# Optimization experiments

Hardware: AMD Instinct MI355X
Metric: run time of the kernel (lower is better)

The kernel has to match this reference:

```python
import jax, jax.numpy as jnp
import numpy as np

ENTRY_SIZE = 8192
TUPLE_SIZE = 16
N_NEURONS = ENTRY_SIZE // TUPLE_SIZE            # 512
ADDR_SPACE = 2 ** TUPLE_SIZE                     # 65536
BATCH = 4096


def setup_inputs() -> dict:
    key = jax.random.key(0)
    k1, k2, k3 = jax.random.split(key, 3)
    # Binary input bits [B, entry_size]
    inp = jax.random.randint(k1, (BATCH, ENTRY_SIZE), 0, 2, dtype=jnp.int32)
    # Permutation mapping bits -> tuples (identity permutation; arange fill)
    tuple_mapping = jnp.arange(ENTRY_SIZE, dtype=jnp.int64)
    # Dense RAM tables emulating the per-neuron dicts:
    #   counts[n, a] = number of training samples that hit address a in neuron n
    #                  (0 means the address was never trained -> not in dict)
    #   sums[n, a]   = accumulated target sum for that address
    counts = jax.random.randint(k2, (N_NEURONS, ADDR_SPACE), 0, 4, dtype=jnp.int32)
    sums = jax.random.normal(k3, (N_NEURONS, ADDR_SPACE), dtype=jnp.float32)
    return {"input": inp, "tuple_mapping": tuple_mapping, "counts": counts, "sums": sums}


def reference(input, tuple_mapping, counts, sums):
    """RegressionWisard.predict with centrality='mean'.

    input:  [B, entry_size] binary bits (int32)
    tuple_mapping: [entry_size] permutation (int)
    counts: [n_neurons, 2^tuple_size] int32 RAM hit counts
    sums:   [n_neurons, 2^tuple_size] float32 RAM target sums
    """
    B = input.shape[0]
    # Map and group bits into tuples: [B, N, T]
    mapped = jnp.take(input, tuple_mapping, axis=1).reshape(B, N_NEURONS, TUPLE_SIZE)
    # Binary address per (sample, neuron); tidx flips so bit 0 is the MSB.
    pow2 = (jnp.int32(1) << jnp.arange(TUPLE_SIZE - 1, -1, -1, dtype=jnp.int32))
    addr = jnp.einsum("bnt,t->bn", mapped, pow2)  # [B, N], values in [0, 2^T)
    neuron_idx = jnp.arange(N_NEURONS, dtype=jnp.int32)[None, :]  # [1, N]
    c = counts[neuron_idx, addr]  # [B, N]
    s = sums[neuron_idx, addr]    # [B, N]
    trained = c > 0               # dict-membership (torch.isin) equivalent
    response = jnp.sum(jnp.where(trained, s, jnp.float32(0)), axis=1)      # [B]
    counters = jnp.sum(jnp.where(trained, c, 0), axis=1).astype(s.dtype)   # [B]
    return jnp.nan_to_num(response / counters)
```

## Files before the change

kernel.cpp:

```cpp
#include <hip/hip_runtime.h>


constexpr int BATCH   = 4096;
constexpr int ENTRY   = 8192;
constexpr int TUP     = 16;
constexpr int NEUR    = ENTRY / TUP;
constexpr int THREADS = 256;
constexpr int SPB     = 2;
constexpr int KPT     = NEUR / THREADS;

typedef int v4i __attribute__((ext_vector_type(4)));

__global__ __launch_bounds__(THREADS) void wisard_kernel(
    const int*   __restrict__ input,
    const int*   __restrict__ mapping,
    const int*   __restrict__ counts,
    const float* __restrict__ sums,
    float*       __restrict__ out)
{
    __shared__ float s_resp[SPB][THREADS / 64];
    __shared__ int   s_cnt [SPB][THREADS / 64];

    const int tid  = threadIdx.x;
    const int lane = tid & 63;
    const int wv   = tid >> 6;
    const int b0   = blockIdx.x * SPB;

    int   cv[SPB][KPT];
    float sv[SPB][KPT];

    #pragma unroll
    for (int k = 0; k < KPT; ++k) {
        const int n = tid + k * THREADS;
        const int* map_n = mapping + n * TUP;

        const int m0 = map_n[0];
        bool contig = ((m0 & 3) == 0);
        #pragma unroll
        for (int t = 1; t < TUP; ++t) contig &= (map_n[t] == m0 + t);

        int addr[SPB];
        if (contig) {
            #pragma unroll
            for (int s = 0; s < SPB; ++s) {
                const v4i* p = reinterpret_cast<const v4i*>(
                    input + (size_t)(b0 + s) * ENTRY + m0);
                const v4i w0 = __builtin_nontemporal_load(p);
                const v4i w1 = __builtin_nontemporal_load(p + 1);
                const v4i w2 = __builtin_nontemporal_load(p + 2);
                const v4i w3 = __builtin_nontemporal_load(p + 3);
                addr[s] = ((w0.x & 1) << 15) | ((w0.y & 1) << 14)
                        | ((w0.z & 1) << 13) | ((w0.w & 1) << 12)
                        | ((w1.x & 1) << 11) | ((w1.y & 1) << 10)
                        | ((w1.z & 1) <<  9) | ((w1.w & 1) <<  8)
                        | ((w2.x & 1) <<  7) | ((w2.y & 1) <<  6)
                        | ((w2.z & 1) <<  5) | ((w2.w & 1) <<  4)
                        | ((w3.x & 1) <<  3) | ((w3.y & 1) <<  2)
                        | ((w3.z & 1) <<  1) |  (w3.w & 1);
            }
        } else {
            #pragma unroll
            for (int s = 0; s < SPB; ++s) {
                const int* row = input + (size_t)(b0 + s) * ENTRY;
                int a = 0;
                #pragma unroll
                for (int t = 0; t < TUP; ++t) a = (a << 1) | (row[map_n[t]] & 1);
                addr[s] = a;
            }
        }

        #pragma unroll
        for (int s = 0; s < SPB; ++s) {
            const size_t idx = ((size_t)n << 16) | (unsigned)addr[s];
            cv[s][k] = counts[idx];
            sv[s][k] = sums  [idx];
        }
    }

    float resp[SPB];
    int   cnt [SPB];
    #pragma unroll
    for (int s = 0; s < SPB; ++s) {
        resp[s] = 0.0f; cnt[s] = 0;
        #pragma unroll
        for (int k = 0; k < KPT; ++k) {
            const bool tr = cv[s][k] > 0;
            resp[s] += tr ? sv[s][k] : 0.0f;
            cnt [s] += tr ? cv[s][k] : 0;
        }
    }

    #pragma unroll
    for (int s = 0; s < SPB; ++s) {
        float r = resp[s]; int c = cnt[s];
        #pragma unroll
        for (int off = 32; off > 0; off >>= 1) {
            r += __shfl_down(r, off, 64);
            c += __shfl_down(c, off, 64);
        }
        if (lane == 0) { s_resp[s][wv] = r; s_cnt[s][wv] = c; }
    }
    __syncthreads();
    if (tid < SPB) {
        float r = 0.0f; int c = 0;
        #pragma unroll
        for (int w = 0; w < THREADS / 64; ++w) { r += s_resp[tid][w]; c += s_cnt[tid][w]; }
        out[b0 + tid] = (c > 0) ? (r / (float)c) : 0.0f;
    }
}

extern "C" void kernel_launch(void* const* d_in, const int* in_sizes, int n_in,
                              void* d_out, int out_size, void* d_ws, size_t ws_size,
                              hipStream_t stream) {
    (void)in_sizes; (void)n_in; (void)out_size; (void)d_ws; (void)ws_size;
    const int*   input   = (const int*)d_in[0];
    const int*   mapping = (const int*)d_in[1];
    const int*   counts  = (const int*)d_in[2];
    const float* sums    = (const float*)d_in[3];
    float*       out     = (float*)d_out;

    wisard_kernel<<<BATCH / SPB, THREADS, 0, stream>>>(input, mapping, counts, sums, out);
}
```

Before: 365.4 us.

## Remap threads to samples per neuron chunk with two-pass partial reduction

The work is re-partitioned so that each block covers 64 samples by 64 neurons. Lanes index samples and waves index groups of 16 neurons, which makes the neuron index and mapping reads wave-uniform. Each block writes partial sums and counts to the workspace, and a second finalize kernel combines the 8 neuron chunks and does the division. The aim is better locality and scalarization of the per-neuron table accesses. The cost is input loads strided by a full row across lanes, an extra kernel launch, and a workspace round trip.

```diff
diff --git a/kernel.cpp b/kernel.cpp
--- a/kernel.cpp
+++ b/kernel.cpp
@@ -6,32 +6,37 @@
 constexpr int TUP     = 16;
 constexpr int NEUR    = ENTRY / TUP;
 constexpr int THREADS = 256;
-constexpr int SPB     = 2;
-constexpr int KPT     = NEUR / THREADS;
+constexpr int NC      = 8;
+constexpr int SC      = BATCH / 64;
+constexpr int NPT     = 16;
 
 typedef int v4i __attribute__((ext_vector_type(4)));
 
-__global__ __launch_bounds__(THREADS) void wisard_kernel(
+__global__ __launch_bounds__(THREADS) void wisard_gather(
     const int*   __restrict__ input,
     const int*   __restrict__ mapping,
     const int*   __restrict__ counts,
     const float* __restrict__ sums,
-    float*       __restrict__ out)
+    float*       __restrict__ part_r,
+    int*         __restrict__ part_c)
 {
-    __shared__ float s_resp[SPB][THREADS / 64];
-    __shared__ int   s_cnt [SPB][THREADS / 64];
+    __shared__ float sr [4][64];
+    __shared__ int   scn[4][64];
 
     const int tid  = threadIdx.x;
     const int lane = tid & 63;
-    const int wv   = tid >> 6;
-    const int b0   = blockIdx.x * SPB;
+    const int w    = tid >> 6;
+    const int nc   = blockIdx.x & (NC - 1);
+    const int sc   = blockIdx.x >> 3;
+    const int s    = sc * 64 + lane;
+    const int nb   = nc * 64 + w * NPT;
 
-    int   cv[SPB][KPT];
-    float sv[SPB][KPT];
+    int   cv[NPT];
+    float sv[NPT];
 
     #pragma unroll
-    for (int k = 0; k < KPT; ++k) {
-        const int n = tid + k * THREADS;
+    for (int i = 0; i < NPT; ++i) {
+        const int n = __builtin_amdgcn_readfirstlane(nb) + i;
         const int* map_n = mapping + n * TUP;
 
         const int m0 = map_n[0];
@@ -39,85 +44,82 @@
         #pragma unroll
         for (int t = 1; t < TUP; ++t) contig &= (map_n[t] == m0 + t);
 
-        int addr[SPB];
+        int addr;
         if (contig) {
+            const v4i* p = reinterpret_cast<const v4i*>(
+                input + (size_t)s * ENTRY + m0);
+            const v4i a0 = __builtin_nontemporal_load(p);
+            const v4i a1 = __builtin_nontemporal_load(p + 1);
+            const v4i a2 = __builtin_nontemporal_load(p + 2);
+            const v4i a3 = __builtin_nontemporal_load(p + 3);
+            addr = ((a0.x & 1) << 15) | ((a0.y & 1) << 14)
+                 | ((a0.z & 1) << 13) | ((a0.w & 1) << 12)
+                 | ((a1.x & 1) << 11) | ((a1.y & 1) << 10)
+                 | ((a1.z & 1) <<  9) | ((a1.w & 1) <<  8)
+                 | ((a2.x & 1) <<  7) | ((a2.y & 1) <<  6)
+                 | ((a2.z & 1) <<  5) | ((a2.w & 1) <<  4)
+                 | ((a3.x & 1) <<  3) | ((a3.y & 1) <<  2)
+                 | ((a3.z & 1) <<  1) |  (a3.w & 1);
+        } else {
+            const int* row = input + (size_t)s * ENTRY;
+            int a = 0;
             #pragma unroll
-            for (int s = 0; s < SPB; ++s) {
-                const v4i* p = reinterpret_cast<const v4i*>(
-                    input + (size_t)(b0 + s) * ENTRY + m0);
-                const v4i w0 = __builtin_nontemporal_load(p);
-                const v4i w1 = __builtin_nontemporal_load(p + 1);
-                const v4i w2 = __builtin_nontemporal_load(p + 2);
-                const v4i w3 = __builtin_nontemporal_load(p + 3);
-                addr[s] = ((w0.x & 1) << 15) | ((w0.y & 1) << 14)
-                        | ((w0.z & 1) << 13) | ((w0.w & 1) << 12)
-                        | ((w1.x & 1) << 11) | ((w1.y & 1) << 10)
-                        | ((w1.z & 1) <<  9) | ((w1.w & 1) <<  8)
-                        | ((w2.x & 1) <<  7) | ((w2.y & 1) <<  6)
-                        | ((w2.z & 1) <<  5) | ((w2.w & 1) <<  4)
-                        | ((w3.x & 1) <<  3) | ((w3.y & 1) <<  2)
-                        | ((w3.z & 1) <<  1) |  (w3.w & 1);
-            }
-        } else {
-            #pragma unroll
-            for (int s = 0; s < SPB; ++s) {
-                const int* row = input + (size_t)(b0 + s) * ENTRY;
-                int a = 0;
-                #pragma unroll
-                for (int t = 0; t < TUP; ++t) a = (a << 1) | (row[map_n[t]] & 1);
-                addr[s] = a;
-            }
+            for (int t = 0; t < TUP; ++t) a = (a << 1) | (row[map_n[t]] & 1);
+            addr = a;
         }
 
-        #pragma unroll
-        for (int s = 0; s < SPB; ++s) {
-            const size_t idx = ((size_t)n << 16) | (unsigned)addr[s];
-            cv[s][k] = counts[idx];
-            sv[s][k] = sums  [idx];
-        }
+        const size_t idx = ((size_t)n << 16) | (unsigned)addr;
+        cv[i] = counts[idx];
+        sv[i] = sums  [idx];
     }
 
-    float resp[SPB];
-    int   cnt [SPB];
+    float r = 0.0f; int c = 0;
     #pragma unroll
-    for (int s = 0; s < SPB; ++s) {
-        resp[s] = 0.0f; cnt[s] = 0;
-        #pragma unroll
-        for (int k = 0; k < KPT; ++k) {
-            const bool tr = cv[s][k] > 0;
-            resp[s] += tr ? sv[s][k] : 0.0f;
-            cnt [s] += tr ? cv[s][k] : 0;
-        }
+    for (int i = 0; i < NPT; ++i) {
+        const bool t = cv[i] > 0;
+        r += t ? sv[i] : 0.0f;
+        c += t ? cv[i] : 0;
     }
 
+    sr[w][lane] = r; scn[w][lane] = c;
+    __syncthreads();
+    if (w == 0) {
+        r = sr[0][lane] + sr[1][lane] + sr[2][lane] + sr[3][lane];
+        c = scn[0][lane] + scn[1][lane] + scn[2][lane] + scn[3][lane];
+        part_r[nc * BATCH + s] = r;
+        part_c[nc * BATCH + s] = c;
+    }
+}
+
+__global__ __launch_bounds__(THREADS) void wisard_finalize(
+    const float* __restrict__ part_r,
+    const int*   __restrict__ part_c,
+    float*       __restrict__ out)
+{
+    const int s = blockIdx.x * THREADS + threadIdx.x;
+    float r = 0.0f; int c = 0;
     #pragma unroll
-    for (int s = 0; s < SPB; ++s) {
-        float r = resp[s]; int c = cnt[s];
-        #pragma unroll
-        for (int off = 32; off > 0; off >>= 1) {
-            r += __shfl_down(r, off, 64);
-            c += __shfl_down(c, off, 64);
-        }
-        if (lane == 0) { s_resp[s][wv] = r; s_cnt[s][wv] = c; }
+    for (int nc = 0; nc < NC; ++nc) {
+        r += part_r[nc * BATCH + s];
+        c += part_c[nc * BATCH + s];
     }
-    __syncthreads();
-    if (tid < SPB) {
-        float r = 0.0f; int c = 0;
-        #pragma unroll
-        for (int w = 0; w < THREADS / 64; ++w) { r += s_resp[tid][w]; c += s_cnt[tid][w]; }
-        out[b0 + tid] = (c > 0) ? (r / (float)c) : 0.0f;
-    }
+    out[s] = (c > 0) ? (r / (float)c) : 0.0f;
 }
 
 extern "C" void kernel_launch(void* const* d_in, const int* in_sizes, int n_in,
                               void* d_out, int out_size, void* d_ws, size_t ws_size,
                               hipStream_t stream) {
-    (void)in_sizes; (void)n_in; (void)out_size; (void)d_ws; (void)ws_size;
+    (void)in_sizes; (void)n_in; (void)out_size; (void)ws_size;
     const int*   input   = (const int*)d_in[0];
     const int*   mapping = (const int*)d_in[1];
     const int*   counts  = (const int*)d_in[2];
     const float* sums    = (const float*)d_in[3];
     float*       out     = (float*)d_out;
 
-    wisard_kernel<<<BATCH / SPB, THREADS, 0, stream>>>(input, mapping, counts, sums, out);
+    float* part_r = (float*)d_ws;
+    int*   part_c = (int*)((char*)d_ws + (size_t)NC * BATCH * sizeof(float));
+
+    wisard_gather<<<SC * NC, THREADS, 0, stream>>>(
+        input, mapping, counts, sums, part_r, part_c);
+    wisard_finalize<<<BATCH / THREADS, THREADS, 0, stream>>>(part_r, part_c, out);
 }
```

Result: slower. 398.4 us (+9.1%).
